# Kernel tuning notes

Hardware: AMD Instinct MI355X
Metric: run time of the kernel (lower is better)

The kernel has to match this reference:

```python
import jax, jax.numpy as jnp
import numpy as np

N_NODES = 16384   # total nodes
B = 32            # graphs in batch
NPG = 512         # nodes per graph (uniform -> dense mask is all True)
E = 262144        # edges (avg degree 16)
H = 64            # hidden_dim
HEADS = 8
DH = H // HEADS


def setup_inputs() -> dict:
    key = jax.random.key(0)
    ks = jax.random.split(key, 20)
    x = jax.random.normal(ks[0], (N_NODES, H), dtype=jnp.float32)
    # edges constrained within each graph of 512 nodes
    src = jax.random.randint(ks[1], (E,), 0, N_NODES, dtype=jnp.int32)
    dst = (src // NPG) * NPG + jax.random.randint(ks[2], (E,), 0, NPG, dtype=jnp.int32)
    edge_index = jnp.stack([src, dst])
    batch = (jnp.arange(N_NODES, dtype=jnp.int32) // NPG)
    c_size = jnp.full((B,), NPG, dtype=jnp.int32)
    s = 1.0 / np.sqrt(H)
    p = lambda k, shape: (jax.random.normal(k, shape, dtype=jnp.float32) * s)
    return {
        "x": x,
        "w_gat": p(ks[3], (H, H)), "att_src": p(ks[4], (H,)), "att_dst": p(ks[5], (H,)), "b_gat": jnp.zeros((H,), jnp.float32),
        "g1": jnp.ones((H,), jnp.float32), "b1": jnp.zeros((H,), jnp.float32),
        "wq": p(ks[6], (H, H)), "bq": jnp.zeros((H,), jnp.float32),
        "wk": p(ks[7], (H, H)), "bk": jnp.zeros((H,), jnp.float32),
        "wv": p(ks[8], (H, H)), "bv": jnp.zeros((H,), jnp.float32),
        "wo": p(ks[9], (H, H)), "bo": jnp.zeros((H,), jnp.float32),
        "g2": jnp.ones((H,), jnp.float32), "b2": jnp.zeros((H,), jnp.float32),
        "edge_index": edge_index, "batch": batch, "c_size": c_size,
    }


def _layer_norm(x, g, b):
    mu = jnp.mean(x, axis=-1, keepdims=True)
    var = jnp.var(x, axis=-1, keepdims=True)
    return (x - mu) * jax.lax.rsqrt(var + 1e-5) * g + b


def _gat_conv(x, edge_index, w, a_src, a_dst, bias):
    # PyG GATConv, 1 head, add_self_loops=True, leaky_relu slope 0.2
    n = x.shape[0]
    loops = jnp.arange(n, dtype=edge_index.dtype)
    src = jnp.concatenate([edge_index[0], loops])
    dst = jnp.concatenate([edge_index[1], loops])
    h = x @ w                                  # [n, H]
    e = jax.nn.leaky_relu((h @ a_src)[src] + (h @ a_dst)[dst], 0.2)  # [E+n]
    m = jax.ops.segment_max(e, dst, num_segments=n)
    p = jnp.exp(e - m[dst])
    s = jax.ops.segment_sum(p, dst, num_segments=n)
    alpha = p / (s[dst] + 1e-16)
    out = jax.ops.segment_sum(alpha[:, None] * h[src], dst, num_segments=n)
    return out + bias


def reference(x, w_gat, att_src, att_dst, b_gat, g1, b1,
              wq, bq, wk, bk, wv, bv, wo, bo, g2, b2,
              edge_index, batch, c_size):
    # GAT branch (dropout is identity in eval)
    x_ = jax.nn.relu(_gat_conv(x, edge_index, w_gat, att_src, att_dst, b_gat))
    x1 = _layer_norm(x + x_, g1, b1)                     # [n, H]
    # to_dense_batch: uniform graphs -> mask all True, plain reshape
    xd = x1.reshape(B, NPG, H)
    q = (xd @ wq + bq).reshape(B, NPG, HEADS, DH)
    k = (xd @ wk + bk).reshape(B, NPG, HEADS, DH)
    v = (xd @ wv + bv).reshape(B, NPG, HEADS, DH)
    scores = jnp.einsum('bqhd,bkhd->bhqk', q, k) / np.sqrt(DH)  # [B,h,N,N]
    attn = jax.nn.softmax(scores, axis=-1)
    o = jnp.einsum('bhqk,bkhd->bqhd', attn, v).reshape(B, NPG, H)
    o = o @ wo + bo
    x2 = _layer_norm(x1 + jax.nn.relu(o.reshape(N_NODES, H)), g2, b2)
    return x2  # recon_loss is None in eval mode
```

## Files before the change

### kernel.cpp

```cpp
#include <hip/hip_runtime.h>
#include <hip/hip_bf16.h>
#include <hip/hip_fp16.h>

#define NN     16384
#define HD     64
#define BG     32
#define NPG    512
#define NHEADS 8
#define DH     8
#define DEGMAX 40

#define QS_STR 12
#define KS_STR 12
#define VT_STR 264

typedef __hip_bfloat16 bf16;
typedef _Float16 v4h __attribute__((ext_vector_type(4)));
typedef float v16f __attribute__((ext_vector_type(16)));

#if defined(__has_builtin)
#if __has_builtin(__builtin_amdgcn_exp2f)
#define EXP2F(x) __builtin_amdgcn_exp2f(x)
#else
#define EXP2F(x) exp2f(x)
#endif
#if __has_builtin(__builtin_amdgcn_fdot2)
#define HAS_FDOT2 1
#endif
#else
#define EXP2F(x) exp2f(x)
#endif

#ifdef HAS_FDOT2
typedef _Float16 hvec2 __attribute__((ext_vector_type(2)));
#endif

__device__ __forceinline__ float fdot2u(unsigned a, unsigned b, float c) {
#ifdef HAS_FDOT2
  union { unsigned u; hvec2 v; } x, y;
  x.u = a; y.u = b;
  return __builtin_amdgcn_fdot2(x.v, y.v, c, false);
#else
  union { unsigned u; __half2 h; } x, y;
  x.u = a; y.u = b;
  return fmaf(__low2float(x.h), __low2float(y.h),
              fmaf(__high2float(x.h), __high2float(y.h), c));
#endif
}

__device__ __forceinline__ float b2f(bf16 v) { return __bfloat162float(v); }

__device__ __forceinline__ float ldf(const void* p, int i, int bf) {
  return bf ? __bfloat162float(((const bf16*)p)[i]) : ((const float*)p)[i];
}

__device__ __forceinline__ float wave_sum(float v) {
#pragma unroll
  for (int off = 32; off > 0; off >>= 1) v += __shfl_xor(v, off);
  return v;
}

__device__ __forceinline__ void unpack8(uint4 u, float* f) {
  f[0] = __uint_as_float(u.x << 16); f[1] = __uint_as_float(u.x & 0xffff0000u);
  f[2] = __uint_as_float(u.y << 16); f[3] = __uint_as_float(u.y & 0xffff0000u);
  f[4] = __uint_as_float(u.z << 16); f[5] = __uint_as_float(u.z & 0xffff0000u);
  f[6] = __uint_as_float(u.w << 16); f[7] = __uint_as_float(u.w & 0xffff0000u);
}

__device__ __forceinline__ unsigned short bfbits(float f) {
  bf16 b = __float2bfloat16(f);
  return *(unsigned short*)&b;
}

__device__ __forceinline__ unsigned packh2(float a, float b) {
  union { unsigned u; __half2 h; } z;
  z.h = __floats2half2_rn(a, b);
  return z.u;
}

__device__ __forceinline__ int detect_bf(const unsigned short* xr, int tid, int nt) {
  __shared__ int s_cnt;
  if (tid == 0) s_cnt = 0;
  __syncthreads();
  int sane = 0;
  for (int i = tid; i < 256; i += nt) {
    int e = (xr[2 * i] >> 7) & 0xFF;
    sane += (e >= 100 && e <= 150) ? 1 : 0;
  }
  if (sane) atomicAdd(&s_cnt, sane);
  __syncthreads();
  return s_cnt > 180;
}

__global__ __launch_bounds__(256) void k_build(
    const void* __restrict__ x, const void* __restrict__ w,
    const void* __restrict__ asrc, const void* __restrict__ adst,
    const int* __restrict__ esrc, const int* __restrict__ edst, int E,
    int* __restrict__ cur, int* __restrict__ ell,
    bf16* __restrict__ h, float* __restrict__ as_, float* __restrict__ ad_,
    int* __restrict__ flagp)
{
  const int tid = threadIdx.x, lane = tid & 63, wid = tid >> 6;
  const int bf = detect_bf((const unsigned short*)x, tid, 256);
  if (tid == 0 && blockIdx.x == 0) *flagp = bf;
  __shared__ float wl[HD * HD];
  __shared__ float xr[4][HD];
  {
    for (int e = blockIdx.x * 256 + tid; e < E; e += gridDim.x * 256) {
      int d = edst[e];
      int k = atomicAdd(&cur[d], 1);
      if (k < DEGMAX) ell[d * DEGMAX + k] = esrc[e];
    }
  }
  for (int i = tid; i < HD * HD; i += 256) wl[i] = ldf(w, i, bf);
  const float av = ldf(asrc, lane, bf), dv_ = ldf(adst, lane, bf);
  __syncthreads();
#pragma unroll
  for (int r = 0; r < 4; ++r) {
    const int node = blockIdx.x * 16 + r * 4 + wid;
    xr[wid][lane] = ldf(x, node * HD + lane, bf);
    float hj = 0.f;
#pragma unroll
    for (int i = 0; i < HD; ++i) hj = fmaf(xr[wid][i], wl[i * HD + lane], hj);
    float pa = wave_sum(hj * av);
    float pd = wave_sum(hj * dv_);
    h[node * HD + lane] = __float2bfloat16(hj);
    if (lane == 0) { as_[node] = pa; ad_[node] = pd; }
  }
}

__global__ __launch_bounds__(256) void k_gather(
    const void* __restrict__ x, const int* __restrict__ cur,
    const int* __restrict__ ell, const float* __restrict__ as_,
    const float* __restrict__ ad_, const bf16* __restrict__ h,
    const void* __restrict__ bg, const void* __restrict__ g1,
    const void* __restrict__ b1,
    const void* __restrict__ wq, const void* __restrict__ bq,
    const void* __restrict__ wk, const void* __restrict__ bk,
    const void* __restrict__ wv, const void* __restrict__ bv,
    const int* __restrict__ dflag,
    unsigned* __restrict__ wpk, float* __restrict__ bpk,
    __half* __restrict__ x1)
{
  const int tid = threadIdx.x, lane = tid & 63, wid = tid >> 6;
  const int bf = *dflag;
  if (blockIdx.x < 4) {
    for (int idx = blockIdx.x * 256 + tid; idx < 3 * 32 * 64; idx += 1024) {
      int m = idx >> 11;
      int r = idx & 2047;
      int kp = r >> 6, col = r & 63;
      const void* ws = (m == 0) ? wq : (m == 1) ? wk : wv;
      wpk[idx] = packh2(ldf(ws, (2 * kp) * HD + col, bf),
                        ldf(ws, (2 * kp + 1) * HD + col, bf));
    }
  } else if (blockIdx.x == 4 && tid < 192) {
    int m = tid >> 6, col = tid & 63;
    const void* bs = (m == 0) ? bq : (m == 1) ? bk : bv;
    bpk[tid] = ldf(bs, col, bf);
  }
  const int n = blockIdx.x * 4 + wid;
  const float adn = ad_[n];
  float e0 = as_[n] + adn;
  e0 = e0 > 0.f ? e0 : 0.2f * e0;
  float den = __expf(fminf(e0, 30.f));
  float num = den * b2f(h[n * HD + lane]);
  const int deg = min(cur[n], DEGMAX);
  const int* row = ell + n * DEGMAX;
  int i = 0;
  for (; i + 8 <= deg; i += 8) {
    int s[8];
#pragma unroll
    for (int k = 0; k < 8; ++k) s[k] = row[i + k];
    float a[8], hh[8];
#pragma unroll
    for (int k = 0; k < 8; ++k) a[k] = as_[s[k]];
#pragma unroll
    for (int k = 0; k < 8; ++k) hh[k] = b2f(h[s[k] * HD + lane]);
#pragma unroll
    for (int k = 0; k < 8; ++k) {
      float e = a[k] + adn;
      e = e > 0.f ? e : 0.2f * e;
      float p = __expf(fminf(e, 30.f));
      den += p;
      num = fmaf(p, hh[k], num);
    }
  }
  for (; i + 4 <= deg; i += 4) {
    int s0 = row[i], s1 = row[i + 1], s2 = row[i + 2], s3 = row[i + 3];
    float a0 = as_[s0], a1 = as_[s1], a2 = as_[s2], a3 = as_[s3];
    float h0 = b2f(h[s0 * HD + lane]), h1 = b2f(h[s1 * HD + lane]);
    float h2 = b2f(h[s2 * HD + lane]), h3 = b2f(h[s3 * HD + lane]);
    float e_0 = a0 + adn; e_0 = e_0 > 0.f ? e_0 : 0.2f * e_0;
    float e_1 = a1 + adn; e_1 = e_1 > 0.f ? e_1 : 0.2f * e_1;
    float e_2 = a2 + adn; e_2 = e_2 > 0.f ? e_2 : 0.2f * e_2;
    float e_3 = a3 + adn; e_3 = e_3 > 0.f ? e_3 : 0.2f * e_3;
    float p0 = __expf(fminf(e_0, 30.f)), p1 = __expf(fminf(e_1, 30.f));
    float p2 = __expf(fminf(e_2, 30.f)), p3 = __expf(fminf(e_3, 30.f));
    den += p0 + p1 + p2 + p3;
    num = fmaf(p0, h0, num); num = fmaf(p1, h1, num);
    num = fmaf(p2, h2, num); num = fmaf(p3, h3, num);
  }
  for (; i < deg; ++i) {
    int s = row[i];
    float e = as_[s] + adn;
    e = e > 0.f ? e : 0.2f * e;
    float p = __expf(fminf(e, 30.f));
    den += p;
    num = fmaf(p, b2f(h[s * HD + lane]), num);
  }
  float v = num / (den + 1e-16f) + ldf(bg, lane, bf);
  v = fmaxf(v, 0.f) + ldf(x, n * HD + lane, bf);
  float mu = wave_sum(v) * (1.f / 64.f);
  float dv = v - mu;
  float var = wave_sum(dv * dv) * (1.f / 64.f);
  float r = rsqrtf(var + 1e-5f);
  x1[n * HD + lane] =
      __float2half(dv * r * ldf(g1, lane, bf) + ldf(b1, lane, bf));
}

__global__ __launch_bounds__(512, 2) void k_attn13(
    const __half* __restrict__ x1,
    const unsigned* __restrict__ wpk, const float* __restrict__ bpk,
    bf16* __restrict__ num_t, float* __restrict__ den_t)
{
  const int t = threadIdx.x;
  __shared__ _Float16 Qs[NPG * QS_STR];
  __shared__ _Float16 Ks[256 * KS_STR];
  __shared__ _Float16 Vt[DH * VT_STR];
  const int bid = blockIdx.x;
  const int g = bid >> 4, hd = (bid >> 1) & 7, half = bid & 1;
  const float qscale = 0.3535533905932738f * 1.4426950408889634f;
  {
    const int r = t & 255;
    const int m = (t < 256) ? 1 : 2;
    const uint4* xk4 = (const uint4*)(x1 + (size_t)(g * NPG + half * 256 + r) * HD);
    const unsigned* wb0 = wpk + m * 2048 + hd * 8;
    float acc[DH];
#pragma unroll
    for (int j = 0; j < DH; ++j) acc[j] = bpk[m * 64 + hd * 8 + j];
#pragma unroll
    for (int blk = 0; blk < 8; ++blk) {
      uint4 xp = xk4[blk];
      const unsigned* wb = wb0 + blk * 256;
#pragma unroll
      for (int j = 0; j < DH; ++j) {
        acc[j] = fdot2u(xp.x, wb[j], acc[j]);
        acc[j] = fdot2u(xp.y, wb[64 + j], acc[j]);
        acc[j] = fdot2u(xp.z, wb[128 + j], acc[j]);
        acc[j] = fdot2u(xp.w, wb[192 + j], acc[j]);
      }
    }
    if (t < 256) {
      unsigned w0 = packh2(acc[0], acc[1]), w1 = packh2(acc[2], acc[3]);
      unsigned w2 = packh2(acc[4], acc[5]), w3 = packh2(acc[6], acc[7]);
      *(uint2*)(Ks + r * KS_STR) = make_uint2(w0, w1);
      *(uint2*)(Ks + r * KS_STR + 4) = make_uint2(w2, w3);
    } else {
#pragma unroll
      for (int j = 0; j < DH; ++j) Vt[j * VT_STR + r] = (_Float16)acc[j];
    }
  }
  {
    const uint4* xa4 = (const uint4*)(x1 + (size_t)(g * NPG + t) * HD);
    const unsigned* wb0 = wpk + hd * 8;
    float qa[DH];
#pragma unroll
    for (int j = 0; j < DH; ++j) qa[j] = bpk[hd * 8 + j];
#pragma unroll
    for (int blk = 0; blk < 8; ++blk) {
      uint4 xp = xa4[blk];
      const unsigned* wb = wb0 + blk * 256;
#pragma unroll
      for (int j = 0; j < DH; ++j) {
        qa[j] = fdot2u(xp.x, wb[j], qa[j]);
        qa[j] = fdot2u(xp.y, wb[64 + j], qa[j]);
        qa[j] = fdot2u(xp.z, wb[128 + j], qa[j]);
        qa[j] = fdot2u(xp.w, wb[192 + j], qa[j]);
      }
    }
    unsigned w0 = packh2(qa[0] * qscale, qa[1] * qscale);
    unsigned w1 = packh2(qa[2] * qscale, qa[3] * qscale);
    unsigned w2 = packh2(qa[4] * qscale, qa[5] * qscale);
    unsigned w3 = packh2(qa[6] * qscale, qa[7] * qscale);
    *(uint2*)(Qs + t * QS_STR) = make_uint2(w0, w1);
    *(uint2*)(Qs + t * QS_STR + 4) = make_uint2(w2, w3);
  }
  __syncthreads();
  const int lane = t & 63, wid = t >> 6;
  const int ln = lane & 31, hh = lane >> 5;
  const int plane = half * 8 + hd;
  const size_t obase = (size_t)plane * NN + (size_t)g * NPG;
  v16f zf;
#pragma unroll
  for (int i = 0; i < 16; ++i) zf[i] = 0.f;
#pragma unroll
  for (int qt = 0; qt < 2; ++qt) {
    const int qbase = (wid * 2 + qt) * 32;
    v4h qf = *(const v4h*)(Qs + (qbase + ln) * QS_STR + 4 * hh);
    v16f oacc = zf;
    float den = 0.f;
#pragma unroll
    for (int kt = 0; kt < 8; ++kt) {
      v4h kf = *(const v4h*)(Ks + (kt * 32 + ln) * KS_STR + 4 * hh);
      v16f s = __builtin_amdgcn_mfma_f32_32x32x8f16(kf, qf, zf, 0, 0, 0);
#pragma unroll
      for (int g2 = 0; g2 < 4; ++g2) {
        float e0 = EXP2F(s[4 * g2 + 0]);
        float e1 = EXP2F(s[4 * g2 + 1]);
        float e2 = EXP2F(s[4 * g2 + 2]);
        float e3 = EXP2F(s[4 * g2 + 3]);
        den += (e0 + e1) + (e2 + e3);
        union { unsigned u[2]; v4h v; } pu;
        pu.u[0] = packh2(e0, e1);
        pu.u[1] = packh2(e2, e3);
        v4h vf = *(const v4h*)(Vt + (ln & 7) * VT_STR + kt * 32 + g2 * 8 + 4 * hh);
        oacc = __builtin_amdgcn_mfma_f32_32x32x8f16(pu.v, vf, oacc, 0, 0, 0);
      }
    }
    den += __shfl_xor(den, 32);
    if (lane < 32) den_t[obase + qbase + lane] = den;
#pragma unroll
    for (int r = 0; r < 16; ++r) {
      const int q = qbase + (r & 3) + 8 * (r >> 2) + 4 * hh;
      if (ln < 8)
        num_t[(obase + q) * 8 + ln] = __float2bfloat16(oacc[r]);
    }
  }
}

__global__ __launch_bounds__(256) void k_out(
    const bf16* __restrict__ num_t, const float* __restrict__ den_t,
    const __half* __restrict__ x1,
    const void* __restrict__ wo, const void* __restrict__ bo,
    const void* __restrict__ g2, const void* __restrict__ b2,
    const int* __restrict__ dflag, void* __restrict__ out)
{
  const int tid = threadIdx.x, lane = tid & 63, wid = tid >> 6;
  const int bf = *dflag;
  __shared__ float wl[HD * HD];
  __shared__ float orow[4][HD];
  for (int i = tid; i < HD * HD; i += 256) wl[i] = ldf(wo, i, bf);
  const float bov = ldf(bo, lane, bf);
  const float g2v = ldf(g2, lane, bf);
  const float b2v = ldf(b2, lane, bf);
  const int hdp = lane >> 3, jp = lane & 7;
  __syncthreads();
#pragma unroll
  for (int r = 0; r < 8; ++r) {
    const int node = blockIdx.x * 32 + r * 4 + wid;
    {
      float nm = b2f(num_t[((size_t)hdp * NN + node) * 8 + jp]) +
                 b2f(num_t[((size_t)(8 + hdp) * NN + node) * 8 + jp]);
      float dn = den_t[(size_t)hdp * NN + node] +
                 den_t[(size_t)(8 + hdp) * NN + node];
      orow[wid][lane] = nm / dn;
    }
    float y = bov;
#pragma unroll
    for (int i = 0; i < HD; ++i) y = fmaf(orow[wid][i], wl[i * HD + lane], y);
    float tt = __half2float(x1[node * HD + lane]) + fmaxf(y, 0.f);
    float mu = wave_sum(tt) * (1.f / 64.f);
    float dv = tt - mu;
    float var = wave_sum(dv * dv) * (1.f / 64.f);
    float rr = rsqrtf(var + 1e-5f);
    float res = dv * rr * g2v + b2v;
    if (bf) ((bf16*)out)[node * HD + lane] = __float2bfloat16(res);
    else    ((float*)out)[node * HD + lane] = res;
  }
}

extern "C" void kernel_launch(void* const* d_in, const int* in_sizes, int n_in,
                              void* d_out, int out_size, void* d_ws, size_t ws_size,
                              hipStream_t stream)
{
  const void* x    = d_in[0];
  const void* wgat = d_in[1];
  const void* asrc = d_in[2];
  const void* adst = d_in[3];
  const void* bgat = d_in[4];
  const void* g1   = d_in[5];
  const void* b1   = d_in[6];
  const void* wq   = d_in[7];
  const void* bq   = d_in[8];
  const void* wk   = d_in[9];
  const void* bk   = d_in[10];
  const void* wv   = d_in[11];
  const void* bv   = d_in[12];
  const void* wo   = d_in[13];
  const void* bo   = d_in[14];
  const void* g2   = d_in[15];
  const void* b2   = d_in[16];
  const int*  ei   = (const int*)d_in[17];
  const int E = in_sizes[17] / 2;
  const int* esrc = ei;
  const int* edst = ei + E;

  char* W = (char*)d_ws;
  __half* x1b  = (__half*)W;
  int*   ell   = (int*)(W + (size_t)(2 << 20));
  bf16*  hb    = (bf16*)(W + (size_t)(2 << 20) + (size_t)NN * DEGMAX * 4);
  bf16*  num_t = (bf16*)(W + (size_t)(2 << 20));
  float* den_t = (float*)(W + (size_t)(6 << 20));
  float* as_   = (float*)(W + (size_t)(7 << 20));
  float* ad_   = as_ + NN;
  int*   cur   = (int*)(ad_ + NN);
  int*   flag  = cur + NN;
  unsigned* wpk = (unsigned*)(flag + 1);
  float* bpk   = (float*)(wpk + 3 * 32 * 64);

  hipMemsetAsync(cur, 0, NN * sizeof(int), stream);
  k_build  <<<NN / 16, 256, 0, stream>>>(x, wgat, asrc, adst, esrc, edst, E,
                                         cur, ell, hb, as_, ad_, flag);
  k_gather <<<NN / 4, 256, 0, stream>>>(x, cur, ell, as_, ad_, hb,
                                        bgat, g1, b1,
                                        wq, bq, wk, bk, wv, bv,
                                        flag, wpk, bpk, x1b);
  k_attn13 <<<BG * NHEADS * 2, 512, 0, stream>>>(x1b, wpk, bpk, num_t, den_t);
  k_out    <<<NN / 32, 256, 0, stream>>>(num_t, den_t, x1b, wo, bo, g2, b2,
                                         flag, d_out);
}
```

Baseline: 180.1 us.

## Compute output projection in k_out with MFMA instead of scalar FMA loop

```diff
diff --git a/kernel.cpp b/kernel.cpp
--- a/kernel.cpp
+++ b/kernel.cpp
@@ -328,44 +328,78 @@
   }
 }
 
-__global__ __launch_bounds__(256) void k_out(
+__global__ __launch_bounds__(64) void k_out(
     const bf16* __restrict__ num_t, const float* __restrict__ den_t,
     const __half* __restrict__ x1,
     const void* __restrict__ wo, const void* __restrict__ bo,
     const void* __restrict__ g2, const void* __restrict__ b2,
     const int* __restrict__ dflag, void* __restrict__ out)
 {
-  const int tid = threadIdx.x, lane = tid & 63, wid = tid >> 6;
+  const int t = threadIdx.x;
   const int bf = *dflag;
-  __shared__ float wl[HD * HD];
-  __shared__ float orow[4][HD];
-  for (int i = tid; i < HD * HD; i += 256) wl[i] = ldf(wo, i, bf);
-  const float bov = ldf(bo, lane, bf);
-  const float g2v = ldf(g2, lane, bf);
-  const float b2v = ldf(b2, lane, bf);
-  const int hdp = lane >> 3, jp = lane & 7;
-  __syncthreads();
-#pragma unroll
-  for (int r = 0; r < 8; ++r) {
-    const int node = blockIdx.x * 32 + r * 4 + wid;
-    {
-      float nm = b2f(num_t[((size_t)hdp * NN + node) * 8 + jp]) +
-                 b2f(num_t[((size_t)(8 + hdp) * NN + node) * 8 + jp]);
-      float dn = den_t[(size_t)hdp * NN + node] +
-                 den_t[(size_t)(8 + hdp) * NN + node];
-      orow[wid][lane] = nm / dn;
-    }
-    float y = bov;
-#pragma unroll
-    for (int i = 0; i < HD; ++i) y = fmaf(orow[wid][i], wl[i * HD + lane], y);
-    float tt = __half2float(x1[node * HD + lane]) + fmaxf(y, 0.f);
-    float mu = wave_sum(tt) * (1.f / 64.f);
-    float dv = tt - mu;
-    float var = wave_sum(dv * dv) * (1.f / 64.f);
-    float rr = rsqrtf(var + 1e-5f);
-    float res = dv * rr * g2v + b2v;
-    if (bf) ((bf16*)out)[node * HD + lane] = __float2bfloat16(res);
-    else    ((float*)out)[node * HD + lane] = res;
+  const int ln = t & 31, hh = t >> 5;
+  const int base = blockIdx.x * 32;
+  const int n = base + ln;
+  v16f c0, c1;
+#pragma unroll
+  for (int i = 0; i < 16; ++i) { c0[i] = 0.f; c1[i] = 0.f; }
+#pragma unroll
+  for (int kt = 0; kt < 8; ++kt) {
+    union { uint2 u; unsigned short s[4]; } L, H;
+    L.u = *(const uint2*)(num_t + ((size_t)kt * NN + n) * 8 + 4 * hh);
+    H.u = *(const uint2*)(num_t + ((size_t)(8 + kt) * NN + n) * 8 + 4 * hh);
+    float den = den_t[(size_t)kt * NN + n] + den_t[(size_t)(8 + kt) * NN + n];
+    float rden = 1.f / den;
+    float o0 = (__uint_as_float((unsigned)L.s[0] << 16) +
+                __uint_as_float((unsigned)H.s[0] << 16)) * rden;
+    float o1 = (__uint_as_float((unsigned)L.s[1] << 16) +
+                __uint_as_float((unsigned)H.s[1] << 16)) * rden;
+    float o2 = (__uint_as_float((unsigned)L.s[2] << 16) +
+                __uint_as_float((unsigned)H.s[2] << 16)) * rden;
+    float o3 = (__uint_as_float((unsigned)L.s[3] << 16) +
+                __uint_as_float((unsigned)H.s[3] << 16)) * rden;
+    union { unsigned u[2]; v4h v; } A;
+    A.u[0] = packh2(o0, o1);
+    A.u[1] = packh2(o2, o3);
+    const int kr = kt * 8 + 4 * hh;
+    union { unsigned u[2]; v4h v; } B0, B1;
+    B0.u[0] = packh2(ldf(wo, (kr + 0) * HD + ln, bf),
+                     ldf(wo, (kr + 1) * HD + ln, bf));
+    B0.u[1] = packh2(ldf(wo, (kr + 2) * HD + ln, bf),
+                     ldf(wo, (kr + 3) * HD + ln, bf));
+    B1.u[0] = packh2(ldf(wo, (kr + 0) * HD + 32 + ln, bf),
+                     ldf(wo, (kr + 1) * HD + 32 + ln, bf));
+    B1.u[1] = packh2(ldf(wo, (kr + 2) * HD + 32 + ln, bf),
+                     ldf(wo, (kr + 3) * HD + 32 + ln, bf));
+    c0 = __builtin_amdgcn_mfma_f32_32x32x8f16(A.v, B0.v, c0, 0, 0, 0);
+    c1 = __builtin_amdgcn_mfma_f32_32x32x8f16(A.v, B1.v, c1, 0, 0, 0);
+  }
+  const float bo0 = ldf(bo, ln, bf),      bo1 = ldf(bo, 32 + ln, bf);
+  const float g20 = ldf(g2, ln, bf),      g21 = ldf(g2, 32 + ln, bf);
+  const float b20 = ldf(b2, ln, bf),      b21 = ldf(b2, 32 + ln, bf);
+#pragma unroll
+  for (int r = 0; r < 16; ++r) {
+    const int node = base + (r & 3) + 8 * (r >> 2) + 4 * hh;
+    float t0 = __half2float(x1[node * HD + ln]) + fmaxf(c0[r] + bo0, 0.f);
+    float t1 = __half2float(x1[node * HD + 32 + ln]) + fmaxf(c1[r] + bo1, 0.f);
+    float s = t0 + t1;
+#pragma unroll
+    for (int off = 1; off < 32; off <<= 1) s += __shfl_xor(s, off);
+    const float mu = s * (1.f / 64.f);
+    const float d0 = t0 - mu, d1 = t1 - mu;
+    float v = d0 * d0 + d1 * d1;
+#pragma unroll
+    for (int off = 1; off < 32; off <<= 1) v += __shfl_xor(v, off);
+    const float rr = rsqrtf(v * (1.f / 64.f) + 1e-5f);
+    const float r0 = d0 * rr * g20 + b20;
+    const float r1 = d1 * rr * g21 + b21;
+    if (bf) {
+      ((bf16*)out)[node * HD + ln]      = __float2bfloat16(r0);
+      ((bf16*)out)[node * HD + 32 + ln] = __float2bfloat16(r1);
+    } else {
+      ((float*)out)[node * HD + ln]      = r0;
+      ((float*)out)[node * HD + 32 + ln] = r1;
+    }
   }
 }
 
@@ -416,6 +450,6 @@
                                         wq, bq, wk, bk, wv, bv,
                                         flag, wpk, bpk, x1b);
   k_attn13 <<<BG * NHEADS * 2, 512, 0, stream>>>(x1b, wpk, bpk, num_t, den_t);
-  k_out    <<<NN / 32, 256, 0, stream>>>(num_t, den_t, x1b, wo, bo, g2, b2,
-                                         flag, d_out);
-}
+  k_out    <<<NN / 32, 64, 0, stream>>>(num_t, den_t, x1b, wo, bo, g2, b2,
+                                        flag, d_out);
+}
```

After: 177.7 us. Within noise of the previous version (-1.3%).
